# Performance work log

Measured on AMD Instinct MI355X. Metric: run time of the kernel, lower is better.

The kernel has to match this reference:

```python
import jax, jax.numpy as jnp
import numpy as np

N = 50000     # num_nodes
E = 600000    # num_edges
H = 128       # h_dim
OUT = 32      # out_dim
R = 64        # num_rels
B = 16        # num_bases


def setup_inputs() -> dict:
    key = jax.random.key(0)
    ks = jax.random.split(key, 11)
    src = jax.random.randint(ks[0], (E,), 0, N)
    dst = jax.random.randint(ks[1], (E,), 0, N)
    etype = jax.random.randint(ks[2], (E,), 0, R)
    norm = jax.random.uniform(ks[3], (E, 1), dtype=jnp.float32)  # edge norm (e.g. 1/deg)
    emb = jax.random.normal(ks[4], (N, H), dtype=jnp.float32) * 0.05
    # basis-decomposed relation weights: W_r = sum_b comp[r,b] * V[b]
    V1 = jax.random.normal(ks[5], (B, H, H), dtype=jnp.float32) * (1.0 / np.sqrt(H))
    comp1 = jax.random.normal(ks[6], (R, B), dtype=jnp.float32) * (1.0 / np.sqrt(B))
    bias1 = jnp.zeros((H,), dtype=jnp.float32)
    V2 = jax.random.normal(ks[7], (B, H, OUT), dtype=jnp.float32) * (1.0 / np.sqrt(H))
    comp2 = jax.random.normal(ks[8], (R, B), dtype=jnp.float32) * (1.0 / np.sqrt(B))
    bias2 = jnp.zeros((OUT,), dtype=jnp.float32)
    return {"src": src, "dst": dst, "etype": etype, "norm": norm, "emb": emb,
            "V1": V1, "comp1": comp1, "bias1": bias1,
            "V2": V2, "comp2": comp2, "bias2": bias2}


def _rel_graph_conv(x, src, dst, etype, norm, V, comp, bias):
    # message for edge e: (x[src_e] @ W_{etype_e}) * norm_e, W_r = sum_b comp[r,b] V_b.
    # Since W is linear, fold norm into the gathered features, and aggregate
    # per (dst, basis) BEFORE the dense basis matmul (aggregate-first trick):
    #   agg[v, b] = sum_{e: dst_e=v} comp[etype_e, b] * norm_e * x[src_e]
    #   out[v]    = sum_b agg[v, b] @ V_b + bias
    xs = x[src] * norm                      # [E, in]
    w = comp[etype]                         # [E, B] per-edge basis coefficients
    # loop over the small fixed basis count (B=16), reusing the [E, in] buffer
    agg = jnp.stack(
        [jax.ops.segment_sum(xs * w[:, b:b + 1], dst, num_segments=N) for b in range(B)],
        axis=1,
    )                                       # [N, B, in]
    return jnp.einsum('nbi,bio->no', agg, V) + bias


def reference(src, dst, etype, norm, emb, V1, comp1, bias1, V2, comp2, bias2):
    h = _rel_graph_conv(emb, src, dst, etype, norm, V1, comp1, bias1)
    h = jax.nn.relu(h)                      # dropout p=0.0 -> identity
    h = _rel_graph_conv(h, src, dst, etype, norm, V2, comp2, bias2)
    return h
```

## Files before the change

### kernel.cpp

```cpp
#include <hip/hip_runtime.h>
#include <hip/hip_bf16.h>

#define NN 50000
#define EE 600000
#define HH 128
#define OUTD 32
#define RR 64
#define BB 16
#define KK 2048
#define SC_B ((NN + 1023) / 1024)
#define N_CONVW ((HH + OUTD) * KK)
#define N_EMB   (NN * HH / 2)
#define TILEB   262144

typedef short s16x8 __attribute__((ext_vector_type(8)));
typedef float f32x4 __attribute__((ext_vector_type(4)));
typedef float f32x2 __attribute__((ext_vector_type(2)));
typedef unsigned short ushort_t;
typedef unsigned int uint_t;
typedef __attribute__((address_space(3))) uint_t lds_u32;
typedef const __attribute__((address_space(1))) uint_t glb_u32;

__device__ inline ushort_t f_to_bf16(float f){
    __hip_bfloat16 h = __float2bfloat16(f);
    return *reinterpret_cast<ushort_t*>(&h);
}
__device__ inline uint_t pack_bf16x2(float a, float b){
    return (uint_t)f_to_bf16(a) | ((uint_t)f_to_bf16(b) << 16);
}

__global__ void hist_kernel(const int* __restrict__ dst, int* counts){
    int e = blockIdx.x*256 + threadIdx.x;
    if (e < EE) atomicAdd(&counts[dst[e]], 1);
}

__global__ void scan_part(const int* __restrict__ counts, int* __restrict__ tot){
    int b = blockIdx.x, t = threadIdx.x;
    int i0 = b*1024 + t*4;
    int s = 0;
    if (i0 + 3 < NN){
        int4 v = *reinterpret_cast<const int4*>(&counts[i0]);
        s = v.x + v.y + v.z + v.w;
    } else {
        for (int j = 0; j < 4; j++) if (i0 + j < NN) s += counts[i0 + j];
    }
    #pragma unroll
    for (int off = 32; off; off >>= 1) s += __shfl_xor(s, off, 64);
    __shared__ int ws[4];
    if ((t & 63) == 0) ws[t >> 6] = s;
    __syncthreads();
    if (t == 0) tot[b] = ws[0] + ws[1] + ws[2] + ws[3];
}

__global__ void scan_tot(int* tot){
    int t = threadIdx.x;
    int v = (t < SC_B) ? tot[t] : 0;
    int x = v;
    #pragma unroll
    for (int off = 1; off < 64; off <<= 1){
        int y = __shfl_up(x, off, 64);
        if (t >= off) x += y;
    }
    if (t < SC_B) tot[t] = x - v;
}

__global__ void scan_final(const int* __restrict__ counts, const int* __restrict__ tot,
                           int* __restrict__ offsets, int* __restrict__ cursor){
    int b = blockIdx.x, t = threadIdx.x, lane = t & 63, wv = t >> 6;
    int i0 = b*1024 + t*4;
    int v[4]; int s = 0;
    #pragma unroll
    for (int j = 0; j < 4; j++){ v[j] = (i0 + j < NN) ? counts[i0 + j] : 0; s += v[j]; }
    int x = s;
    #pragma unroll
    for (int off = 1; off < 64; off <<= 1){
        int y = __shfl_up(x, off, 64);
        if (lane >= off) x += y;
    }
    __shared__ int ws[4];
    if (lane == 63) ws[wv] = x;
    __syncthreads();
    int pre = tot[b];
    for (int i = 0; i < wv; i++) pre += ws[i];
    int run = pre + x - s;
    #pragma unroll
    for (int j = 0; j < 4; j++){
        if (i0 + j < NN){
            cursor[i0 + j] = run;
            offsets[i0 + j + 1] = run + v[j];
        }
        run += v[j];
    }
    if (b == 0 && t == 0) offsets[0] = 0;
}

__global__ void scatter_kernel(const int* __restrict__ dst, const int* __restrict__ src,
                               const int* __restrict__ etype, const float* __restrict__ norm,
                               int* cursor, int* __restrict__ msrc, int* __restrict__ netn){
    int e = blockIdx.x*256 + threadIdx.x;
    if (e >= EE) return;
    int d = dst[e];
    int r = atomicAdd(&cursor[d], 1);
    msrc[r] = src[e];
    netn[r] = (__float_as_int(norm[e]) & ~63) | etype[e];
}

__global__ void prep_kernel(const float* __restrict__ V1, const float* __restrict__ V2,
                            const float* __restrict__ emb,
                            ushort_t* __restrict__ Wt1, ushort_t* __restrict__ Wt2,
                            ushort_t* __restrict__ xb){
    int i = blockIdx.x*256 + threadIdx.x;
    if (i < HH*KK){
        int o = i / KK, k = i % KK;
        size_t addr = (size_t)(k >> 6)*16384 + (size_t)o*128
                    + ((((k & 63) >> 3) ^ (o & 7)) << 4) + (k & 7)*2;
        *reinterpret_cast<ushort_t*>(reinterpret_cast<char*>(Wt1) + addr) =
            f_to_bf16(V1[(size_t)k*HH + o]);
    } else if (i < N_CONVW){
        int j = i - HH*KK;
        int o = j / KK, k = j % KK;
        size_t addr = (size_t)(k >> 6)*4096 + (size_t)o*128
                    + ((((k & 63) >> 3) ^ (o & 7)) << 4) + (k & 7)*2;
        *reinterpret_cast<ushort_t*>(reinterpret_cast<char*>(Wt2) + addr) =
            f_to_bf16(V2[(size_t)k*OUTD + o]);
    } else if (i < N_CONVW + N_EMB){
        int j = i - N_CONVW;
        float2 f = *reinterpret_cast<const float2*>(emb + 2*(size_t)j);
        *reinterpret_cast<uint_t*>(xb + 2*(size_t)j) = pack_bf16x2(f.x, f.y);
    }
}

__global__ __launch_bounds__(256, 6) void agg_kernel(
    const ushort_t* __restrict__ xin, const int* __restrict__ msrc,
    const int* __restrict__ netn, const int* __restrict__ offsets,
    const float* __restrict__ comp, ushort_t* __restrict__ agg,
    int v0, int vc)
{
    int w = threadIdx.x >> 6, lane = threadIdx.x & 63;
    int v = v0 + blockIdx.x*4 + w;
    if (v >= v0 + vc) return;
    int p0 = offsets[v];
    int dd = offsets[v+1] - p0;
    const uint_t* xrow = reinterpret_cast<const uint_t*>(xin);

    f32x2 accA[8], accB[8];
    #pragma unroll
    for (int bp = 0; bp < 8; bp++){
        accA[bp].x = 0.f; accA[bp].y = 0.f;
        accB[bp].x = 0.f; accB[bp].y = 0.f;
    }

    for (int c0 = 0; c0 < dd; c0 += 64){
        int nc = min(64, dd - c0);
        int li = p0 + c0 + min(lane, nc - 1);
        int mp = msrc[li];
        int nr = netn[li];
        uint_t xr[8];
        #pragma unroll
        for (int j = 0; j < 8; ++j){
            int sr = __builtin_amdgcn_readlane(mp, min(j, nc - 1));
            xr[j] = xrow[(size_t)sr*64 + lane];
        }
        for (int eb = 0; eb < nc; eb += 8){
            #pragma unroll
            for (int j = 0; j < 8; ++j){
                int e = eb + j;
                int ec = min(e, nc - 1);
                int nb = __builtin_amdgcn_readlane(nr, ec);
                int et = nb & 63;
                float nw = (e < nc) ? __int_as_float(nb & ~63) : 0.f;
                uint_t u = xr[j];
                f32x2 xs;
                xs.x = __uint_as_float(u << 16) * nw;
                xs.y = __uint_as_float(u & 0xffff0000u) * nw;
                int en = e + 8;
                if (en < nc){
                    int srn = __builtin_amdgcn_readlane(mp, en);
                    xr[j] = xrow[(size_t)srn*64 + lane];
                }
                const f32x2* cp = reinterpret_cast<const f32x2*>(comp + et*BB);
                #pragma unroll
                for (int bp = 0; bp < 8; bp++){
                    f32x2 c2 = cp[bp];
                    asm("v_pk_fma_f32 %0, %1, %2, %0 op_sel:[0,0,0] op_sel_hi:[1,0,1]"
                        : "+v"(accA[bp]) : "s"(c2), "v"(xs));
                    asm("v_pk_fma_f32 %0, %1, %2, %0 op_sel:[0,1,0] op_sel_hi:[1,1,1]"
                        : "+v"(accB[bp]) : "s"(c2), "v"(xs));
                }
            }
        }
    }
    {
        int idx = v - v0;
        int r = idx & 63;
        char* tbase = reinterpret_cast<char*>(agg) + (size_t)(idx >> 6)*TILEB + r*128;
        int goff = ((((lane & 31) >> 2) ^ (r & 7)) << 4) + (lane & 3)*4;
        #pragma unroll
        for (int b = 0; b < BB; b++){
            uint_t pk;
            asm("v_cvt_pk_bf16_f32 %0, %1, %2"
                : "=v"(pk) : "v"(accA[b>>1][b&1]), "v"(accB[b>>1][b&1]));
            int kc = b*2 + (lane >> 5);
            *reinterpret_cast<uint_t*>(tbase + kc*8192 + goff) = pk;
        }
    }
}

template<int BN, bool RELU, bool OUT_BF16>
__global__ __launch_bounds__(512, 6) void gemm_kernel(
    const ushort_t* __restrict__ A, const ushort_t* __restrict__ Wt,
    const float* __restrict__ bias, void* __restrict__ yout, int vc)
{
    __shared__ __align__(16) char Ald[2][64*128];
    __shared__ __align__(16) char Bld[2][BN*128];
    constexpr int CT = (BN == 128) ? 4 : 1;
    constexpr int NT = KK / 64;
    constexpr int BSTRIDE = BN * 128;
    int tid = threadIdx.x, lane = tid & 63, lane15 = lane & 15;
    int w = tid >> 6;
    int wrbase = (BN == 128) ? (w >> 1)*16 : (w & 3)*16;
    int wcbase = (BN == 128) ? (w & 1)*64 : (w >> 2)*16;
    int m0 = blockIdx.x * 64;

    const char* agp = reinterpret_cast<const char*>(A) + (size_t)blockIdx.x*TILEB
                    + w*1024 + lane*16;
    const char* bgp0 = reinterpret_cast<const char*>(Wt)
                     + ((BN == 128) ? (w*2048) : (w*1024)) + lane*16;
    const char* bgp1 = reinterpret_cast<const char*>(Wt) + w*2048 + 1024 + lane*16;

    auto stage = [&](int buf){
        __builtin_amdgcn_global_load_lds((glb_u32*)agp,
            (lds_u32*)(&Ald[buf][w*1024]), 16, 0, 0);
        agp += 8192;
        if constexpr (BN == 128){
            __builtin_amdgcn_global_load_lds((glb_u32*)bgp0,
                (lds_u32*)(&Bld[buf][w*2048]), 16, 0, 0);
            __builtin_amdgcn_global_load_lds((glb_u32*)bgp1,
                (lds_u32*)(&Bld[buf][w*2048 + 1024]), 16, 0, 0);
            bgp0 += BSTRIDE; bgp1 += BSTRIDE;
        } else {
            if (w < 4){
                __builtin_amdgcn_global_load_lds((glb_u32*)bgp0,
                    (lds_u32*)(&Bld[buf][w*1024]), 16, 0, 0);
                bgp0 += BSTRIDE;
            }
        }
    };

    f32x4 acc[CT];
    #pragma unroll
    for (int ct = 0; ct < CT; ct++)
        #pragma unroll
        for (int j = 0; j < 4; j++) acc[ct][j] = 0.f;

    auto compute = [&](int buf){
        #pragma unroll
        for (int ks = 0; ks < 2; ks++){
            int csw = (ks*4 + (lane >> 4)) ^ (lane15 & 7);
            int arow = wrbase + lane15;
            s16x8 a = *reinterpret_cast<const s16x8*>(&Ald[buf][arow*128 + csw*16]);
            #pragma unroll
            for (int ct = 0; ct < CT; ct++){
                int brow = wcbase + ct*16 + lane15;
                s16x8 b = *reinterpret_cast<const s16x8*>(&Bld[buf][brow*128 + csw*16]);
                acc[ct] = __builtin_amdgcn_mfma_f32_16x16x32_bf16(a, b, acc[ct], 0,0,0);
            }
        }
    };

    stage(0);
    for (int t = 0; t < NT; ++t){
        int cur = t & 1;
        if (t + 1 < NT){
            stage(cur ^ 1);
            if (BN == 128)       asm volatile("s_waitcnt vmcnt(3)" ::: "memory");
            else if (w < 4)      asm volatile("s_waitcnt vmcnt(2)" ::: "memory");
            else                 asm volatile("s_waitcnt vmcnt(1)" ::: "memory");
        } else {
            asm volatile("s_waitcnt vmcnt(0)" ::: "memory");
        }
        __builtin_amdgcn_s_barrier();
        __builtin_amdgcn_sched_barrier(0);
        compute(cur);
        __builtin_amdgcn_s_barrier();
    }

    int rb = m0 + wrbase + ((lane >> 4) << 2);
    #pragma unroll
    for (int ct = 0; ct < CT; ct++){
        int col = wcbase + ct*16 + lane15;
        float bv = bias[col];
        #pragma unroll
        for (int r = 0; r < 4; r++){
            int row = rb + r;
            if (row < vc){
                float val = acc[ct][r] + bv;
                if (RELU) val = fmaxf(val, 0.f);
                if (OUT_BF16)
                    reinterpret_cast<ushort_t*>(yout)[(size_t)row*BN + col] = f_to_bf16(val);
                else
                    reinterpret_cast<float*>(yout)[(size_t)row*BN + col] = val;
            }
        }
    }
}

extern "C" void kernel_launch(void* const* d_in, const int* in_sizes, int n_in,
                              void* d_out, int out_size, void* d_ws, size_t ws_size,
                              hipStream_t stream){
    const int*   src   = (const int*)d_in[0];
    const int*   dst   = (const int*)d_in[1];
    const int*   etype = (const int*)d_in[2];
    const float* norm  = (const float*)d_in[3];
    const float* emb   = (const float*)d_in[4];
    const float* V1    = (const float*)d_in[5];
    const float* comp1 = (const float*)d_in[6];
    const float* bias1 = (const float*)d_in[7];
    const float* V2    = (const float*)d_in[8];
    const float* comp2 = (const float*)d_in[9];
    const float* bias2 = (const float*)d_in[10];
    float* out = (float*)d_out;

    char* w = (char*)d_ws;
    auto alloc = [&](size_t bytes) -> char* {
        char* p = w; w += (bytes + 255) & ~(size_t)255; return p;
    };
    int*      offsets = (int*)alloc((NN + 1) * 4);
    int*      counts  = (int*)alloc(NN * 4);
    int*      cursor  = (int*)alloc(NN * 4);
    int*      tot     = (int*)alloc(SC_B * 4);
    int*      msrc    = (int*)alloc((size_t)EE * 4);
    int*      netn    = (int*)alloc((size_t)EE * 4);
    ushort_t* Wt1     = (ushort_t*)alloc((size_t)HH * KK * 2);
    ushort_t* Wt2     = (ushort_t*)alloc((size_t)OUTD * KK * 2);
    ushort_t* xb      = (ushort_t*)alloc((size_t)NN * HH * 2);
    ushort_t* h       = (ushort_t*)alloc((size_t)NN * HH * 2);
    size_t used  = (size_t)(w - (char*)d_ws);
    size_t avail = ws_size > used ? ws_size - used : 0;
    int chunkN = (int)(avail / ((size_t)KK * 2));
    chunkN &= ~127;
    if (chunkN < 128) chunkN = 128;
    if (chunkN > NN) chunkN = NN;
    ushort_t* agg = (ushort_t*)w;

    hipMemsetAsync(counts, 0, NN * 4, stream);
    hist_kernel<<<(EE + 255)/256, 256, 0, stream>>>(dst, counts);
    scan_part<<<SC_B, 256, 0, stream>>>(counts, tot);
    scan_tot<<<1, 64, 0, stream>>>(tot);
    scan_final<<<SC_B, 256, 0, stream>>>(counts, tot, offsets, cursor);
    scatter_kernel<<<(EE + 255)/256, 256, 0, stream>>>(dst, src, etype, norm,
                                                       cursor, msrc, netn);
    prep_kernel<<<(N_CONVW + N_EMB + 255)/256, 256, 0, stream>>>(
        V1, V2, emb, Wt1, Wt2, xb);

    for (int v0 = 0; v0 < NN; v0 += chunkN){
        int vc = (NN - v0 < chunkN) ? (NN - v0) : chunkN;
        agg_kernel<<<(vc + 3)/4, 256, 0, stream>>>(
            xb, msrc, netn, offsets, comp1, agg, v0, vc);
        gemm_kernel<HH, true, true><<<(vc + 63)/64, 512, 0, stream>>>(
            agg, Wt1, bias1, h + (size_t)v0 * HH, vc);
    }
    for (int v0 = 0; v0 < NN; v0 += chunkN){
        int vc = (NN - v0 < chunkN) ? (NN - v0) : chunkN;
        agg_kernel<<<(vc + 3)/4, 256, 0, stream>>>(
            h, msrc, netn, offsets, comp2, agg, v0, vc);
        gemm_kernel<OUTD, false, false><<<(vc + 63)/64, 512, 0, stream>>>(
            agg, Wt2, bias2, out + (size_t)v0 * OUTD, vc);
    }
}
```

Measured before the change: 304.6 us.

## Replace LDS-staged GEMM with single-wave direct-global-load MFMA kernel

```diff
diff --git a/kernel.cpp b/kernel.cpp
--- a/kernel.cpp
+++ b/kernel.cpp
@@ -18,8 +18,6 @@
 typedef float f32x2 __attribute__((ext_vector_type(2)));
 typedef unsigned short ushort_t;
 typedef unsigned int uint_t;
-typedef __attribute__((address_space(3))) uint_t lds_u32;
-typedef const __attribute__((address_space(1))) uint_t glb_u32;
 
 __device__ inline ushort_t f_to_bf16(float f){
     __hip_bfloat16 h = __float2bfloat16(f);
@@ -112,15 +110,13 @@
     int i = blockIdx.x*256 + threadIdx.x;
     if (i < HH*KK){
         int o = i / KK, k = i % KK;
-        size_t addr = (size_t)(k >> 6)*16384 + (size_t)o*128
-                    + ((((k & 63) >> 3) ^ (o & 7)) << 4) + (k & 7)*2;
+        size_t addr = (size_t)(k >> 6)*16384 + (size_t)o*128 + (k & 63)*2;
         *reinterpret_cast<ushort_t*>(reinterpret_cast<char*>(Wt1) + addr) =
             f_to_bf16(V1[(size_t)k*HH + o]);
     } else if (i < N_CONVW){
         int j = i - HH*KK;
         int o = j / KK, k = j % KK;
-        size_t addr = (size_t)(k >> 6)*4096 + (size_t)o*128
-                    + ((((k & 63) >> 3) ^ (o & 7)) << 4) + (k & 7)*2;
+        size_t addr = (size_t)(k >> 6)*4096 + (size_t)o*128 + (k & 63)*2;
         *reinterpret_cast<ushort_t*>(reinterpret_cast<char*>(Wt2) + addr) =
             f_to_bf16(V2[(size_t)k*OUTD + o]);
     } else if (i < N_CONVW + N_EMB){
@@ -192,114 +188,85 @@
     }
     {
         int idx = v - v0;
-        int r = idx & 63;
-        char* tbase = reinterpret_cast<char*>(agg) + (size_t)(idx >> 6)*TILEB + r*128;
-        int goff = ((((lane & 31) >> 2) ^ (r & 7)) << 4) + (lane & 3)*4;
+        char* tbase = reinterpret_cast<char*>(agg) + (size_t)(idx >> 6)*TILEB
+                    + (size_t)(idx & 63)*128;
+        int off = (lane & 31)*4;
         #pragma unroll
         for (int b = 0; b < BB; b++){
             uint_t pk;
             asm("v_cvt_pk_bf16_f32 %0, %1, %2"
                 : "=v"(pk) : "v"(accA[b>>1][b&1]), "v"(accB[b>>1][b&1]));
             int kc = b*2 + (lane >> 5);
-            *reinterpret_cast<uint_t*>(tbase + kc*8192 + goff) = pk;
+            *reinterpret_cast<uint_t*>(tbase + (size_t)kc*8192 + off) = pk;
         }
     }
 }
 
 template<int BN, bool RELU, bool OUT_BF16>
-__global__ __launch_bounds__(512, 6) void gemm_kernel(
+__global__ __launch_bounds__(64, 4) void gemm_kernel(
     const ushort_t* __restrict__ A, const ushort_t* __restrict__ Wt,
     const float* __restrict__ bias, void* __restrict__ yout, int vc)
 {
-    __shared__ __align__(16) char Ald[2][64*128];
-    __shared__ __align__(16) char Bld[2][BN*128];
-    constexpr int CT = (BN == 128) ? 4 : 1;
-    constexpr int NT = KK / 64;
-    constexpr int BSTRIDE = BN * 128;
-    int tid = threadIdx.x, lane = tid & 63, lane15 = lane & 15;
-    int w = tid >> 6;
-    int wrbase = (BN == 128) ? (w >> 1)*16 : (w & 3)*16;
-    int wcbase = (BN == 128) ? (w & 1)*64 : (w >> 2)*16;
-    int m0 = blockIdx.x * 64;
-
-    const char* agp = reinterpret_cast<const char*>(A) + (size_t)blockIdx.x*TILEB
-                    + w*1024 + lane*16;
-    const char* bgp0 = reinterpret_cast<const char*>(Wt)
-                     + ((BN == 128) ? (w*2048) : (w*1024)) + lane*16;
-    const char* bgp1 = reinterpret_cast<const char*>(Wt) + w*2048 + 1024 + lane*16;
-
-    auto stage = [&](int buf){
-        __builtin_amdgcn_global_load_lds((glb_u32*)agp,
-            (lds_u32*)(&Ald[buf][w*1024]), 16, 0, 0);
-        agp += 8192;
-        if constexpr (BN == 128){
-            __builtin_amdgcn_global_load_lds((glb_u32*)bgp0,
-                (lds_u32*)(&Bld[buf][w*2048]), 16, 0, 0);
-            __builtin_amdgcn_global_load_lds((glb_u32*)bgp1,
-                (lds_u32*)(&Bld[buf][w*2048 + 1024]), 16, 0, 0);
-            bgp0 += BSTRIDE; bgp1 += BSTRIDE;
-        } else {
-            if (w < 4){
-                __builtin_amdgcn_global_load_lds((glb_u32*)bgp0,
-                    (lds_u32*)(&Bld[buf][w*1024]), 16, 0, 0);
-                bgp0 += BSTRIDE;
-            }
-        }
-    };
-
-    f32x4 acc[CT];
-    #pragma unroll
-    for (int ct = 0; ct < CT; ct++)
-        #pragma unroll
-        for (int j = 0; j < 4; j++) acc[ct][j] = 0.f;
-
-    auto compute = [&](int buf){
-        #pragma unroll
-        for (int ks = 0; ks < 2; ks++){
-            int csw = (ks*4 + (lane >> 4)) ^ (lane15 & 7);
-            int arow = wrbase + lane15;
-            s16x8 a = *reinterpret_cast<const s16x8*>(&Ald[buf][arow*128 + csw*16]);
+    constexpr int CT = (BN == 128) ? 4 : 2;
+    constexpr int BROWB = BN * 128;
+    int lane = threadIdx.x;
+    int lane15 = lane & 15;
+    int bid = blockIdx.x;
+    int rg, cb;
+    if (BN == 128){ rg = bid >> 1; cb = (bid & 1)*64; }
+    else          { rg = bid;      cb = 0; }
+    int m0 = rg * 32;
+
+    const char* Ab = reinterpret_cast<const char*>(A)
+                   + (size_t)(m0 >> 6)*TILEB + (size_t)(m0 & 63)*128;
+    const char* Bb = reinterpret_cast<const char*>(Wt);
+    int loff = (lane >> 4)*16;
+
+    f32x4 acc[2][CT];
+    #pragma unroll
+    for (int rt = 0; rt < 2; rt++)
+        #pragma unroll
+        for (int ct = 0; ct < CT; ct++)
+            #pragma unroll
+            for (int j = 0; j < 4; j++) acc[rt][ct][j] = 0.f;
+
+    for (int kc = 0; kc < KK/64; ++kc){
+        #pragma unroll
+        for (int ks = 0; ks < 2; ++ks){
+            s16x8 a0 = *reinterpret_cast<const s16x8*>(
+                Ab + (size_t)(lane15)*128      + ks*64 + loff);
+            s16x8 a1 = *reinterpret_cast<const s16x8*>(
+                Ab + (size_t)(16 + lane15)*128 + ks*64 + loff);
             #pragma unroll
             for (int ct = 0; ct < CT; ct++){
-                int brow = wcbase + ct*16 + lane15;
-                s16x8 b = *reinterpret_cast<const s16x8*>(&Bld[buf][brow*128 + csw*16]);
-                acc[ct] = __builtin_amdgcn_mfma_f32_16x16x32_bf16(a, b, acc[ct], 0,0,0);
+                s16x8 b = *reinterpret_cast<const s16x8*>(
+                    Bb + (size_t)(cb + ct*16 + lane15)*128 + ks*64 + loff);
+                acc[0][ct] = __builtin_amdgcn_mfma_f32_16x16x32_bf16(a0, b, acc[0][ct], 0,0,0);
+                acc[1][ct] = __builtin_amdgcn_mfma_f32_16x16x32_bf16(a1, b, acc[1][ct], 0,0,0);
             }
         }
-    };
-
-    stage(0);
-    for (int t = 0; t < NT; ++t){
-        int cur = t & 1;
-        if (t + 1 < NT){
-            stage(cur ^ 1);
-            if (BN == 128)       asm volatile("s_waitcnt vmcnt(3)" ::: "memory");
-            else if (w < 4)      asm volatile("s_waitcnt vmcnt(2)" ::: "memory");
-            else                 asm volatile("s_waitcnt vmcnt(1)" ::: "memory");
-        } else {
-            asm volatile("s_waitcnt vmcnt(0)" ::: "memory");
-        }
-        __builtin_amdgcn_s_barrier();
-        __builtin_amdgcn_sched_barrier(0);
-        compute(cur);
-        __builtin_amdgcn_s_barrier();
-    }
-
-    int rb = m0 + wrbase + ((lane >> 4) << 2);
-    #pragma unroll
-    for (int ct = 0; ct < CT; ct++){
-        int col = wcbase + ct*16 + lane15;
-        float bv = bias[col];
-        #pragma unroll
-        for (int r = 0; r < 4; r++){
-            int row = rb + r;
-            if (row < vc){
-                float val = acc[ct][r] + bv;
-                if (RELU) val = fmaxf(val, 0.f);
-                if (OUT_BF16)
-                    reinterpret_cast<ushort_t*>(yout)[(size_t)row*BN + col] = f_to_bf16(val);
-                else
-                    reinterpret_cast<float*>(yout)[(size_t)row*BN + col] = val;
+        Ab += 8192;
+        Bb += BROWB;
+    }
+
+    #pragma unroll
+    for (int rt = 0; rt < 2; rt++){
+        int rb = m0 + rt*16 + ((lane >> 4) << 2);
+        #pragma unroll
+        for (int ct = 0; ct < CT; ct++){
+            int col = cb + ct*16 + lane15;
+            float bv = bias[col];
+            #pragma unroll
+            for (int r = 0; r < 4; r++){
+                int row = rb + r;
+                if (row < vc){
+                    float val = acc[rt][ct][r] + bv;
+                    if (RELU) val = fmaxf(val, 0.f);
+                    if (OUT_BF16)
+                        reinterpret_cast<ushort_t*>(yout)[(size_t)row*BN + col] = f_to_bf16(val);
+                    else
+                        reinterpret_cast<float*>(yout)[(size_t)row*BN + col] = val;
+                }
             }
         }
     }
@@ -337,9 +304,9 @@
     ushort_t* h       = (ushort_t*)alloc((size_t)NN * HH * 2);
     size_t used  = (size_t)(w - (char*)d_ws);
     size_t avail = ws_size > used ? ws_size - used : 0;
-    int chunkN = (int)(avail / ((size_t)KK * 2));
-    chunkN &= ~127;
-    if (chunkN < 128) chunkN = 128;
+    int maxTiles = (int)(avail / TILEB);
+    int chunkN = maxTiles * 64;
+    if (chunkN < 64) chunkN = 64;
     if (chunkN > NN) chunkN = NN;
     ushort_t* agg = (ushort_t*)w;
 
@@ -357,14 +324,14 @@
         int vc = (NN - v0 < chunkN) ? (NN - v0) : chunkN;
         agg_kernel<<<(vc + 3)/4, 256, 0, stream>>>(
             xb, msrc, netn, offsets, comp1, agg, v0, vc);
-        gemm_kernel<HH, true, true><<<(vc + 63)/64, 512, 0, stream>>>(
+        gemm_kernel<HH, true, true><<<((vc + 31)/32)*2, 64, 0, stream>>>(
             agg, Wt1, bias1, h + (size_t)v0 * HH, vc);
     }
     for (int v0 = 0; v0 < NN; v0 += chunkN){
         int vc = (NN - v0 < chunkN) ? (NN - v0) : chunkN;
         agg_kernel<<<(vc + 3)/4, 256, 0, stream>>>(
             h, msrc, netn, offsets, comp2, agg, v0, vc);
-        gemm_kernel<OUTD, false, false><<<(vc + 63)/64, 512, 0, stream>>>(
+        gemm_kernel<OUTD, false, false><<<(vc + 31)/32, 64, 0, stream>>>(
             agg, Wt2, bias2, out + (size_t)v0 * OUTD, vc);
     }
 }
```

After: 406.8 us. +33.6%, slower.
